# Kernel tuning notes

Hardware: AMD Instinct MI355X
Metric: run time of the kernel (lower is better)

Reference implementation:

```python
import jax, jax.numpy as jnp
import numpy as np

H, W = 224, 224
NF, IN_NF, NL = 32, 100, 4


def conv2d(x, w):
    # 3x3 same-padding conv, NCHW / OIHW
    return jax.lax.conv_general_dilated(x, w, (1, 1), [(1, 1), (1, 1)],
                                        dimension_numbers=('NCHW', 'OIHW', 'NCHW'))


def prelu(x, a):
    return jnp.where(x >= 0, x, a[None, :, None, None] * x)


def bilinear_warp(x, flow):
    # backward warp: sample x at (grid + flow), border clamping
    B, C, Hh, Ww = x.shape
    yy, xx = jnp.meshgrid(jnp.arange(Hh, dtype=x.dtype), jnp.arange(Ww, dtype=x.dtype), indexing='ij')
    px = xx[None] + flow[:, 0]  # [B,H,W]
    py = yy[None] + flow[:, 1]
    x0 = jnp.floor(px); y0 = jnp.floor(py)
    wx = (px - x0)[:, None]; wy = (py - y0)[:, None]  # [B,1,H,W]
    cx = lambda v: jnp.clip(v, 0, Ww - 1).astype(jnp.int32)
    cy = lambda v: jnp.clip(v, 0, Hh - 1).astype(jnp.int32)
    x0i, x1i = cx(x0), cx(x0 + 1)
    y0i, y1i = cy(y0), cy(y0 + 1)
    gather = jax.vmap(lambda img, yi, xi: img[:, yi, xi])  # per-batch fancy gather -> [C,H,W]
    I00 = gather(x, y0i, x0i); I01 = gather(x, y0i, x1i)
    I10 = gather(x, y1i, x0i); I11 = gather(x, y1i, x1i)
    return I00 * (1 - wx) * (1 - wy) + I01 * wx * (1 - wy) + I10 * (1 - wx) * wy + I11 * wx * wy


def glblock_forward(feat_0, feat_1, feat_dense, flow, space_mask,
                    w_head, a_head, w_blocks, a_blocks, w_last, b_last, w_mask, b_mask):
    f0w = bilinear_warp(feat_0, flow[:, :2])
    f1w = bilinear_warp(feat_1, flow[:, 2:4])
    x = jnp.concatenate([f0w, f1w, feat_dense, flow], axis=1)  # [1, in_nf, H, W]
    mask_up = jnp.repeat(jnp.repeat(space_mask, 2, axis=2), 2, axis=3)
    # head: conv3x3 (no bias) + PReLU, then spatial masking
    x = prelu(conv2d(x, w_head), a_head) * space_mask
    outs = [x]
    for i in range(w_blocks.shape[0]):
        x = prelu(conv2d(x, w_blocks[i]) * space_mask, a_blocks[i])
        outs.append(x)
    feats = jnp.concatenate(outs, axis=1)  # [1, in_nf*(NL+1), H, W]
    x = jnp.einsum('oi,bihw->bohw', w_last, feats) + b_last[None, :, None, None]  # 1x1 conv
    smn = conv2d(x[:, 4:], w_mask) + b_mask[None, :, None, None]  # [1,2,H,W]
    B, C, Hh, Ww = x.shape
    xu = jax.image.resize(x, (B, C, 2 * Hh, 2 * Ww), 'linear')
    smnu = jax.image.resize(smn, (B, 2, 2 * Hh, 2 * Ww), 'linear')
    flow_out = xu[:, :4]
    feat_t = xu[:, 4:]
    # eval-mode hard routing mask (training uses gumbel-softmax)
    mask_next = (smnu[:, :1] > smnu[:, 1:]).astype(x.dtype) * mask_up
    return flow_out, feat_t, mask_next


def setup_inputs() -> dict:
    key = jax.random.key(0)
    ks = jax.random.split(key, 12)
    r = lambda i, shape, s=1.0: jax.random.normal(ks[i], shape, jnp.float32) * s
    return {
        'feat_0': r(0, (1, NF, H, W)),
        'feat_1': r(1, (1, NF, H, W)),
        'feat_dense': r(2, (1, NF, H, W)),
        'flow': r(3, (1, 4, H, W)),
        'space_mask': jax.random.uniform(ks[4], (1, 1, H, W), jnp.float32),
        'w_head': r(5, (IN_NF, IN_NF, 3, 3), 0.02),
        'a_head': jnp.full((IN_NF,), 0.25, jnp.float32),
        'w_blocks': r(6, (NL, IN_NF, IN_NF, 3, 3), 0.02),
        'a_blocks': jnp.full((NL, IN_NF), 0.25, jnp.float32),
        'w_last': r(7, (4 + NF, IN_NF * (NL + 1)), 0.02),
        'b_last': r(8, (4 + NF,), 0.02),
        'w_mask': r(9, (2, NF, 3, 3), 0.02),
        'b_mask': r(10, (2,), 0.02),
    }


def reference(feat_0, feat_1, feat_dense, flow, space_mask,
              w_head, a_head, w_blocks, a_blocks, w_last, b_last, w_mask, b_mask):
    return glblock_forward(feat_0, feat_1, feat_dense, flow, space_mask,
                           w_head, a_head, w_blocks, a_blocks, w_last, b_last, w_mask, b_mask)
```

## Files before the change

### kernel.cpp

```cpp
#include <hip/hip_runtime.h>
#include <hip/hip_bf16.h>

#define HWs 50176
#define WID 224
#define OHW 200704

typedef __attribute__((ext_vector_type(8))) short s16x8;
typedef __attribute__((ext_vector_type(4))) float f32x4;

static __device__ __forceinline__ unsigned short f2bf(float x) {
  unsigned u = __float_as_uint(x);
  unsigned r = (u + 0x7fffu + ((u >> 16) & 1u)) >> 16;
  return (unsigned short)r;
}
static __device__ __forceinline__ float bf2f(unsigned short b) {
  return __uint_as_float(((unsigned)b) << 16);
}

__global__ void k_wt(const float* __restrict__ w_head, const float* __restrict__ w_blk,
                     unsigned short* __restrict__ bw) {
  int gid = blockIdx.x * 256 + threadIdx.x;
  int frag = gid >> 7, rr = gid & 127;
  int spl = rr >> 6, lane = rr & 63;
  int l = frag / 288, q = frag - l * 288;
  int t = q / 32, q2 = q - t * 32;
  int ck = q2 >> 3, nt = q2 & 7;
  int oc = nt * 16 + (lane & 15);
  int kg = lane >> 4;
  const float* src = (l == 0) ? w_head : (w_blk + (size_t)(l - 1) * 90000);
  s16x8 outv;
  #pragma unroll
  for (int e = 0; e < 8; ++e) {
    int ic = ck * 32 + kg * 8 + e;
    float w = (oc < 100 && ic < 100) ? src[oc * 900 + ic * 9 + t] : 0.f;
    unsigned short h = f2bf(w);
    unsigned short lo = f2bf(w - bf2f(h));
    outv[e] = (short)(spl ? lo : h);
  }
  ((s16x8*)bw)[gid] = outv;
}

__global__ void k_wlT(const float* __restrict__ wlast, float* __restrict__ wlT) {
  int i = blockIdx.x * 256 + threadIdx.x;
  if (i < 18000) {
    int il = i / 36, o = i - il * 36;
    wlT[i] = wlast[o * 500 + il];
  }
}

__global__ void k_binit(const float* __restrict__ blast, float* __restrict__ xlast) {
  int p = blockIdx.x * 256 + threadIdx.x;
  xlast[(size_t)blockIdx.y * HWs + p] = blast[blockIdx.y];
}

__global__ void k_warp(const float* __restrict__ f0, const float* __restrict__ f1,
                       const float* __restrict__ fd, const float* __restrict__ fl,
                       float* __restrict__ xin) {
  int p = blockIdx.x * 256 + threadIdx.x;
  int yq = blockIdx.y;
  int y = p / WID, x = p - y * WID;
  float fx0 = fl[p];
  float fy0 = fl[HWs + p];
  float fx1 = fl[2 * HWs + p];
  float fy1 = fl[3 * HWs + p];

  #pragma unroll
  for (int img = 0; img < 2; ++img) {
    const float* src = img ? f1 : f0;
    float fx = img ? fx1 : fx0;
    float fy = img ? fy1 : fy0;
    float px = (float)x + fx, py = (float)y + fy;
    float x0f = floorf(px), y0f = floorf(py);
    float wx = px - x0f, wy = py - y0f;
    int x0 = (int)fminf(fmaxf(x0f,       0.f), 223.f);
    int x1 = (int)fminf(fmaxf(x0f + 1.f, 0.f), 223.f);
    int y0 = (int)fminf(fmaxf(y0f,       0.f), 223.f);
    int y1 = (int)fminf(fmaxf(y0f + 1.f, 0.f), 223.f);
    float w00 = (1.f - wx) * (1.f - wy), w01 = wx * (1.f - wy);
    float w10 = (1.f - wx) * wy,         w11 = wx * wy;
    int i00 = y0 * WID + x0, i01 = y0 * WID + x1;
    int i10 = y1 * WID + x0, i11 = y1 * WID + x1;
    float* dst = xin + img * 32 * HWs;
    for (int c = yq * 8; c < yq * 8 + 8; ++c) {
      const float* pl = src + c * HWs;
      dst[c * HWs + p] = w00 * pl[i00] + w01 * pl[i01]
                       + w10 * pl[i10] + w11 * pl[i11];
    }
  }
  for (int c = yq * 8; c < yq * 8 + 8; ++c)
    xin[(64 + c) * HWs + p] = fd[c * HWs + p];
  if (yq == 0) {
    xin[96 * HWs + p] = fx0; xin[97 * HWs + p] = fy0;
    xin[98 * HWs + p] = fx1; xin[99 * HWs + p] = fy1;
  }
}

__global__ __launch_bounds__(256) void k_conv(
    const float* __restrict__ in, const unsigned short* __restrict__ bw,
    const float* __restrict__ avec, const float* __restrict__ mask,
    float* __restrict__ out) {
  __shared__ __align__(16) unsigned char sh[2][6 * 34 * 160];
  const int tid = threadIdx.x;
  const int lane = tid & 63;
  const int wv = tid >> 6;
  const int wr = wv >> 1, wz = wv & 1;
  const int c0 = blockIdx.x * 32;
  const int r0 = blockIdx.y * 4;
  const int li = lane & 15, kg = lane >> 4;

  f32x4 acc[4][4];
  #pragma unroll
  for (int a = 0; a < 4; ++a)
    #pragma unroll
    for (int b = 0; b < 4; ++b) acc[a][b] = (f32x4){0.f, 0.f, 0.f, 0.f};

  const s16x8* bp = (const s16x8*)bw;
  s16x8 bcur[4][2], bnxt[4][2];
  #pragma unroll
  for (int nt = 0; nt < 4; ++nt)
    #pragma unroll
    for (int sp = 0; sp < 2; ++sp)
      bnxt[nt][sp] = bp[(((wz * 4 + nt) * 2 + sp) << 6) + lane];

  auto STAGE = [&](int ck, unsigned char* dst) {
    for (int j = tid; j < 816; j += 256) {
      int kgs = j & 3;
      int rc = j >> 2;
      int pr = rc / 34, pc = rc - pr * 34;
      int gy = r0 - 1 + pr, gx = c0 - 1 + pc;
      int gb = ck * 32 + kgs * 8;
      bool inb = ((unsigned)gy < 224u) && ((unsigned)gx < 224u);
      const float* src = in + (size_t)gb * HWs + gy * WID + gx;
      s16x8 hv, lv;
      #pragma unroll
      for (int e = 0; e < 8; ++e) {
        float v = 0.f;
        if (inb && (gb + e) < 100) v = src[(size_t)e * HWs];
        unsigned short h = f2bf(v);
        unsigned short l2 = f2bf(v - bf2f(h));
        hv[e] = (short)h; lv[e] = (short)l2;
      }
      int base = rc * 160, sw = (rc & 7) << 4;
      *(s16x8*)(dst + base + ((kgs * 16) ^ sw)) = hv;
      *(s16x8*)(dst + base + ((64 + kgs * 16) ^ sw)) = lv;
    }
  };

  STAGE(0, sh[0]);
  __syncthreads();

  for (int ck = 0; ck < 4; ++ck) {
    unsigned char* cur = sh[ck & 1];
    if (ck < 3) STAGE(ck + 1, sh[(ck + 1) & 1]);

    #pragma unroll
    for (int t = 0; t < 9; ++t) {
      #pragma unroll
      for (int nt = 0; nt < 4; ++nt) {
        bcur[nt][0] = bnxt[nt][0];
        bcur[nt][1] = bnxt[nt][1];
      }
      if (t < 8 || ck < 3) {
        int nf = (t < 8) ? (t + 1) * 32 + ck * 8 : (ck + 1) * 8;
        #pragma unroll
        for (int nt = 0; nt < 4; ++nt)
          #pragma unroll
          for (int sp = 0; sp < 2; ++sp)
            bnxt[nt][sp] = bp[(((nf + wz * 4 + nt) * 2 + sp) << 6) + lane];
      }
      const int dy = t / 3 - 1, dx = t - (t / 3) * 3 - 1;
      #pragma unroll
      for (int ms = 0; ms < 4; ++ms) {
        int pr = wr * 2 + (ms >> 1) + 1 + dy;
        int pc = (ms & 1) * 16 + li + 1 + dx;
        int rc = pr * 34 + pc;
        int base = rc * 160, sw = (rc & 7) << 4;
        s16x8 ah = *(const s16x8*)(cur + base + ((kg * 16) ^ sw));
        s16x8 al = *(const s16x8*)(cur + base + ((64 + kg * 16) ^ sw));
        #pragma unroll
        for (int nt = 0; nt < 4; ++nt) {
          acc[ms][nt] = __builtin_amdgcn_mfma_f32_16x16x32_bf16(ah, bcur[nt][0], acc[ms][nt], 0, 0, 0);
          acc[ms][nt] = __builtin_amdgcn_mfma_f32_16x16x32_bf16(al, bcur[nt][0], acc[ms][nt], 0, 0, 0);
          acc[ms][nt] = __builtin_amdgcn_mfma_f32_16x16x32_bf16(ah, bcur[nt][1], acc[ms][nt], 0, 0, 0);
        }
      }
    }
    __syncthreads();
  }

  float4 mv[4];
  #pragma unroll
  for (int ms = 0; ms < 4; ++ms) {
    int row = r0 + wr * 2 + (ms >> 1);
    int colb = c0 + (ms & 1) * 16 + kg * 4;
    mv[ms] = *(const float4*)&mask[row * WID + colb];
  }
  #pragma unroll
  for (int nt = 0; nt < 4; ++nt) {
    int oc = wz * 64 + nt * 16 + li;
    if (oc < 100) {
      float a = avec[oc];
      #pragma unroll
      for (int ms = 0; ms < 4; ++ms) {
        int row = r0 + wr * 2 + (ms >> 1);
        int colb = c0 + (ms & 1) * 16 + kg * 4;
        f32x4 zv = acc[ms][nt];
        float4 o;
        o.x = (zv.x >= 0.f ? zv.x : a * zv.x) * mv[ms].x;
        o.y = (zv.y >= 0.f ? zv.y : a * zv.y) * mv[ms].y;
        o.z = (zv.z >= 0.f ? zv.z : a * zv.z) * mv[ms].z;
        o.w = (zv.w >= 0.f ? zv.w : a * zv.w) * mv[ms].w;
        *(float4*)&out[(size_t)oc * HWs + row * WID + colb] = o;
      }
    }
  }
}

__global__ __launch_bounds__(64) void k_esum(
    const float* __restrict__ A0, const float* __restrict__ A1,
    const float* __restrict__ A2, const float* __restrict__ A3,
    const float* __restrict__ A4, const float* __restrict__ wlT,
    float* __restrict__ xlast) {
  int p = blockIdx.x * 64 + threadIdx.x;
  int l = blockIdx.y;
  const float* a = (l == 0) ? A0 : (l == 1) ? A1 : (l == 2) ? A2 : (l == 3) ? A3 : A4;
  const float* w = wlT + l * 3600;
  float acc[36];
  #pragma unroll
  for (int o = 0; o < 36; ++o) acc[o] = 0.f;
  for (int c0 = 0; c0 < 100; c0 += 10) {
    float v[10];
    #pragma unroll
    for (int q = 0; q < 10; ++q)
      v[q] = a[(size_t)(c0 + q) * HWs + p];
    #pragma unroll
    for (int q = 0; q < 10; ++q) {
      const float4* wp = (const float4*)(w + (c0 + q) * 36);
      #pragma unroll
      for (int j = 0; j < 9; ++j) {
        float4 t = wp[j];
        acc[4*j]   = fmaf(t.x, v[q], acc[4*j]);
        acc[4*j+1] = fmaf(t.y, v[q], acc[4*j+1]);
        acc[4*j+2] = fmaf(t.z, v[q], acc[4*j+2]);
        acc[4*j+3] = fmaf(t.w, v[q], acc[4*j+3]);
      }
    }
  }
  #pragma unroll
  for (int o = 0; o < 36; ++o)
    atomicAdd(&xlast[(size_t)o * HWs + p], acc[o]);
}

__global__ void k_smn(const float* __restrict__ xlast, const float* __restrict__ wmask,
                      const float* __restrict__ bmask, float* __restrict__ smnh) {
  __shared__ float wm[288];
  int tid = threadIdx.x;
  int h = blockIdx.y;
  for (int j = tid; j < 288; j += 64) {
    int o = j / 144, r = j - o * 144;
    wm[j] = wmask[o * 288 + h * 144 + r];
  }
  __syncthreads();
  int p = blockIdx.x * 64 + tid;
  int y = p / WID, x = p - y * WID;
  double a0 = 0.0, a1 = 0.0;
  for (int icl = 0; icl < 16; ++icl) {
    const float* pl = xlast + (size_t)(4 + h * 16 + icl) * HWs;
    #pragma unroll
    for (int dy = -1; dy <= 1; ++dy) {
      int gy = y + dy;
      if ((unsigned)gy < 224u) {
        #pragma unroll
        for (int dx = -1; dx <= 1; ++dx) {
          int gx = x + dx;
          if ((unsigned)gx < 224u) {
            double v = (double)pl[gy * WID + gx];
            int t = (dy + 1) * 3 + (dx + 1);
            a0 += (double)wm[icl * 9 + t] * v;
            a1 += (double)wm[144 + icl * 9 + t] * v;
          }
        }
      }
    }
  }
  if (h == 0) { a0 += (double)bmask[0]; a1 += (double)bmask[1]; }
  smnh[(size_t)(h * 2 + 0) * HWs + p] = (float)a0;
  smnh[(size_t)(h * 2 + 1) * HWs + p] = (float)a1;
}

__global__ void k_upsample(const float* __restrict__ xlast, const float* __restrict__ smnh,
                           const float* __restrict__ smask, float* __restrict__ out) {
  int q = blockIdx.x * 256 + threadIdx.x;
  int oy = q / 448, ox = q - oy * 448;
  int ky = oy >> 1, kx = ox >> 1;
  int r0, r1, c0, c1; float wy0, wy1, wx0, wx1;
  if (oy & 1) { r0 = ky; r1 = (ky < 223) ? ky + 1 : 223; wy0 = 0.75f; wy1 = 0.25f; }
  else        { r0 = (ky > 0) ? ky - 1 : 0; r1 = ky;     wy0 = 0.25f; wy1 = 0.75f; }
  if (ox & 1) { c0 = kx; c1 = (kx < 223) ? kx + 1 : 223; wx0 = 0.75f; wx1 = 0.25f; }
  else        { c0 = (kx > 0) ? kx - 1 : 0; c1 = kx;     wx0 = 0.25f; wx1 = 0.75f; }
  float w00 = wy0 * wx0, w01 = wy0 * wx1, w10 = wy1 * wx0, w11 = wy1 * wx1;
  int i00 = r0 * WID + c0, i01 = r0 * WID + c1, i10 = r1 * WID + c0, i11 = r1 * WID + c1;
  for (int ch = 0; ch < 36; ++ch) {
    const float* pl = xlast + (size_t)ch * HWs;
    out[(size_t)ch * OHW + q] = w00 * pl[i00] + w01 * pl[i01]
                              + w10 * pl[i10] + w11 * pl[i11];
  }
  const float* sa0 = smnh;
  const float* sa1 = smnh + HWs;
  const float* sb0 = smnh + 2 * HWs;
  const float* sb1 = smnh + 3 * HWs;
  double s0 = (double)w00 * ((double)sa0[i00] + (double)sb0[i00])
            + (double)w01 * ((double)sa0[i01] + (double)sb0[i01])
            + (double)w10 * ((double)sa0[i10] + (double)sb0[i10])
            + (double)w11 * ((double)sa0[i11] + (double)sb0[i11]);
  double s1 = (double)w00 * ((double)sa1[i00] + (double)sb1[i00])
            + (double)w01 * ((double)sa1[i01] + (double)sb1[i01])
            + (double)w10 * ((double)sa1[i10] + (double)sb1[i10])
            + (double)w11 * ((double)sa1[i11] + (double)sb1[i11]);
  float mu = smask[ky * WID + kx];
  out[36 * OHW + q] = (s0 > s1) ? mu : 0.f;
}

extern "C" void kernel_launch(void* const* d_in, const int* in_sizes, int n_in,
                              void* d_out, int out_size, void* d_ws, size_t ws_size,
                              hipStream_t stream) {
  const float* feat0   = (const float*)d_in[0];
  const float* feat1   = (const float*)d_in[1];
  const float* featd   = (const float*)d_in[2];
  const float* flow    = (const float*)d_in[3];
  const float* smask   = (const float*)d_in[4];
  const float* w_head  = (const float*)d_in[5];
  const float* a_head  = (const float*)d_in[6];
  const float* w_blk   = (const float*)d_in[7];
  const float* a_blk   = (const float*)d_in[8];
  const float* w_last  = (const float*)d_in[9];
  const float* b_last  = (const float*)d_in[10];
  const float* w_mask  = (const float*)d_in[11];
  const float* b_mask  = (const float*)d_in[12];

  float* B0 = (float*)d_ws;
  float* B1 = B0 + (size_t)100 * HWs;
  float* B2 = B1 + (size_t)100 * HWs;
  float* B3 = B2 + (size_t)100 * HWs;
  float* B4 = B3 + (size_t)100 * HWs;
  float* smnh = B4 + (size_t)100 * HWs;
  float* wlT  = smnh + (size_t)4 * HWs;
  float* xlast = wlT + 18000;
  unsigned short* bw = (unsigned short*)xlast;

  k_wt<<<dim3(720), 256, 0, stream>>>(w_head, w_blk, bw);
  k_wlT<<<dim3(71), 256, 0, stream>>>(w_last, wlT);
  k_warp<<<dim3(196, 4), 256, 0, stream>>>(feat0, feat1, featd, flow, B0);

  dim3 cgrid(7, 56);
  k_conv<<<cgrid, 256, 0, stream>>>(B0, bw,               a_head,      smask, B1);
  k_conv<<<cgrid, 256, 0, stream>>>(B1, bw + 1 * 294912,  a_blk,       smask, B0);
  k_conv<<<cgrid, 256, 0, stream>>>(B0, bw + 2 * 294912,  a_blk + 100, smask, B2);
  k_conv<<<cgrid, 256, 0, stream>>>(B2, bw + 3 * 294912,  a_blk + 200, smask, B3);
  k_conv<<<cgrid, 256, 0, stream>>>(B3, bw + 4 * 294912,  a_blk + 300, smask, B4);

  k_binit<<<dim3(196, 36), 256, 0, stream>>>(b_last, xlast);
  k_esum<<<dim3(784, 5), 64, 0, stream>>>(B1, B0, B2, B3, B4, wlT, xlast);

  k_smn<<<dim3(784, 2), 64, 0, stream>>>(xlast, w_mask, b_mask, smnh);
  k_upsample<<<784, 256, 0, stream>>>(xlast, smnh, smask, (float*)d_out);
}
```

Before: 462.7 us.

## Fuse 1x1 last-conv accumulation into each 3x3 conv epilogue

Each conv layer now stages its activated output tile in shared memory and immediately multiplies it by that layer's slice of the 1x1 last-conv weights, atomically accumulating into xlast. This removes the separate k_esum pass that re-read all five 100-channel activation buffers from global memory, and lets the workspace ping-pong between two buffers. In exchange the conv epilogue does extra FMA work, per-thread global weight loads and 36 atomics per pixel per layer, and uses a larger shared-memory footprint.

```diff
diff --git a/kernel.cpp b/kernel.cpp
--- a/kernel.cpp
+++ b/kernel.cpp
@@ -42,9 +42,10 @@
 
 __global__ void k_wlT(const float* __restrict__ wlast, float* __restrict__ wlT) {
   int i = blockIdx.x * 256 + threadIdx.x;
-  if (i < 18000) {
-    int il = i / 36, o = i - il * 36;
-    wlT[i] = wlast[o * 500 + il];
+  if (i < 18720) {
+    int l = i / 3744, rem = i - l * 3744;
+    int c = rem / 36, o = rem - c * 36;
+    wlT[i] = (c < 100) ? wlast[o * 500 + l * 100 + c] : 0.f;
   }
 }
 
@@ -98,8 +99,9 @@
 __global__ __launch_bounds__(256) void k_conv(
     const float* __restrict__ in, const unsigned short* __restrict__ bw,
     const float* __restrict__ avec, const float* __restrict__ mask,
-    float* __restrict__ out) {
-  __shared__ __align__(16) unsigned char sh[2][6 * 34 * 160];
+    const float* __restrict__ wl, float* __restrict__ out,
+    float* __restrict__ xlast) {
+  __shared__ __align__(16) unsigned char sh[65280];
   const int tid = threadIdx.x;
   const int lane = tid & 63;
   const int wv = tid >> 6;
@@ -146,12 +148,12 @@
     }
   };
 
-  STAGE(0, sh[0]);
+  STAGE(0, sh);
   __syncthreads();
 
   for (int ck = 0; ck < 4; ++ck) {
-    unsigned char* cur = sh[ck & 1];
-    if (ck < 3) STAGE(ck + 1, sh[(ck + 1) & 1]);
+    unsigned char* cur = sh + (ck & 1) * 32640;
+    if (ck < 3) STAGE(ck + 1, sh + ((ck + 1) & 1) * 32640);
 
     #pragma unroll
     for (int t = 0; t < 9; ++t) {
@@ -188,6 +190,7 @@
     __syncthreads();
   }
 
+  float* act = (float*)sh;
   float4 mv[4];
   #pragma unroll
   for (int ms = 0; ms < 4; ++ms) {
@@ -204,6 +207,7 @@
       for (int ms = 0; ms < 4; ++ms) {
         int row = r0 + wr * 2 + (ms >> 1);
         int colb = c0 + (ms & 1) * 16 + kg * 4;
+        int pxb = (wr * 2 + (ms >> 1)) * 32 + (ms & 1) * 16 + kg * 4;
         f32x4 zv = acc[ms][nt];
         float4 o;
         o.x = (zv.x >= 0.f ? zv.x : a * zv.x) * mv[ms].x;
@@ -211,44 +215,51 @@
         o.z = (zv.z >= 0.f ? zv.z : a * zv.z) * mv[ms].z;
         o.w = (zv.w >= 0.f ? zv.w : a * zv.w) * mv[ms].w;
         *(float4*)&out[(size_t)oc * HWs + row * WID + colb] = o;
-      }
-    }
-  }
-}
-
-__global__ __launch_bounds__(64) void k_esum(
-    const float* __restrict__ A0, const float* __restrict__ A1,
-    const float* __restrict__ A2, const float* __restrict__ A3,
-    const float* __restrict__ A4, const float* __restrict__ wlT,
-    float* __restrict__ xlast) {
-  int p = blockIdx.x * 64 + threadIdx.x;
-  int l = blockIdx.y;
-  const float* a = (l == 0) ? A0 : (l == 1) ? A1 : (l == 2) ? A2 : (l == 3) ? A3 : A4;
-  const float* w = wlT + l * 3600;
-  float acc[36];
-  #pragma unroll
-  for (int o = 0; o < 36; ++o) acc[o] = 0.f;
-  for (int c0 = 0; c0 < 100; c0 += 10) {
-    float v[10];
-    #pragma unroll
-    for (int q = 0; q < 10; ++q)
-      v[q] = a[(size_t)(c0 + q) * HWs + p];
-    #pragma unroll
-    for (int q = 0; q < 10; ++q) {
-      const float4* wp = (const float4*)(w + (c0 + q) * 36);
-      #pragma unroll
-      for (int j = 0; j < 9; ++j) {
-        float4 t = wp[j];
-        acc[4*j]   = fmaf(t.x, v[q], acc[4*j]);
-        acc[4*j+1] = fmaf(t.y, v[q], acc[4*j+1]);
-        acc[4*j+2] = fmaf(t.z, v[q], acc[4*j+2]);
-        acc[4*j+3] = fmaf(t.w, v[q], acc[4*j+3]);
-      }
-    }
-  }
+        act[(pxb + 0) * 108 + oc] = o.x;
+        act[(pxb + 1) * 108 + oc] = o.y;
+        act[(pxb + 2) * 108 + oc] = o.z;
+        act[(pxb + 3) * 108 + oc] = o.w;
+      }
+    } else if (oc < 104) {
+      #pragma unroll
+      for (int ms = 0; ms < 4; ++ms) {
+        int pxb = (wr * 2 + (ms >> 1)) * 32 + (ms & 1) * 16 + kg * 4;
+        act[(pxb + 0) * 108 + oc] = 0.f;
+        act[(pxb + 1) * 108 + oc] = 0.f;
+        act[(pxb + 2) * 108 + oc] = 0.f;
+        act[(pxb + 3) * 108 + oc] = 0.f;
+      }
+    }
+  }
+  __syncthreads();
+
+  int px = tid >> 1, h = tid & 1;
+  float ac[36];
+  #pragma unroll
+  for (int o = 0; o < 36; ++o) ac[o] = 0.f;
+  #pragma unroll
+  for (int j = 0; j < 13; ++j) {
+    int c = h * 52 + 4 * j;
+    float4 v4 = *(const float4*)&act[px * 108 + c];
+    float ve[4] = {v4.x, v4.y, v4.z, v4.w};
+    #pragma unroll
+    for (int e = 0; e < 4; ++e) {
+      float v = ve[e];
+      const float4* wp = (const float4*)(wl + (c + e) * 36);
+      #pragma unroll
+      for (int q = 0; q < 9; ++q) {
+        float4 t = wp[q];
+        ac[4*q]   = fmaf(t.x, v, ac[4*q]);
+        ac[4*q+1] = fmaf(t.y, v, ac[4*q+1]);
+        ac[4*q+2] = fmaf(t.z, v, ac[4*q+2]);
+        ac[4*q+3] = fmaf(t.w, v, ac[4*q+3]);
+      }
+    }
+  }
+  int gp = (r0 + (px >> 5)) * WID + c0 + (px & 31);
   #pragma unroll
   for (int o = 0; o < 36; ++o)
-    atomicAdd(&xlast[(size_t)o * HWs + p], acc[o]);
+    atomicAdd(&xlast[(size_t)o * HWs + gp], ac[o]);
 }
 
 __global__ void k_smn(const float* __restrict__ xlast, const float* __restrict__ wmask,
@@ -338,29 +349,24 @@
   const float* w_mask  = (const float*)d_in[11];
   const float* b_mask  = (const float*)d_in[12];
 
-  float* B0 = (float*)d_ws;
-  float* B1 = B0 + (size_t)100 * HWs;
-  float* B2 = B1 + (size_t)100 * HWs;
-  float* B3 = B2 + (size_t)100 * HWs;
-  float* B4 = B3 + (size_t)100 * HWs;
-  float* smnh = B4 + (size_t)100 * HWs;
-  float* wlT  = smnh + (size_t)4 * HWs;
-  float* xlast = wlT + 18000;
-  unsigned short* bw = (unsigned short*)xlast;
+  float* B0    = (float*)d_ws;
+  float* B1    = B0 + (size_t)100 * HWs;
+  float* xlast = B1 + (size_t)100 * HWs;
+  float* smnh  = xlast + (size_t)36 * HWs;
+  float* wlT   = smnh + (size_t)4 * HWs;
+  unsigned short* bw = (unsigned short*)(wlT + 18720);
 
   k_wt<<<dim3(720), 256, 0, stream>>>(w_head, w_blk, bw);
-  k_wlT<<<dim3(71), 256, 0, stream>>>(w_last, wlT);
+  k_wlT<<<dim3(74), 256, 0, stream>>>(w_last, wlT);
+  k_binit<<<dim3(196, 36), 256, 0, stream>>>(b_last, xlast);
   k_warp<<<dim3(196, 4), 256, 0, stream>>>(feat0, feat1, featd, flow, B0);
 
   dim3 cgrid(7, 56);
-  k_conv<<<cgrid, 256, 0, stream>>>(B0, bw,               a_head,      smask, B1);
-  k_conv<<<cgrid, 256, 0, stream>>>(B1, bw + 1 * 294912,  a_blk,       smask, B0);
-  k_conv<<<cgrid, 256, 0, stream>>>(B0, bw + 2 * 294912,  a_blk + 100, smask, B2);
-  k_conv<<<cgrid, 256, 0, stream>>>(B2, bw + 3 * 294912,  a_blk + 200, smask, B3);
-  k_conv<<<cgrid, 256, 0, stream>>>(B3, bw + 4 * 294912,  a_blk + 300, smask, B4);
-
-  k_binit<<<dim3(196, 36), 256, 0, stream>>>(b_last, xlast);
-  k_esum<<<dim3(784, 5), 64, 0, stream>>>(B1, B0, B2, B3, B4, wlT, xlast);
+  k_conv<<<cgrid, 256, 0, stream>>>(B0, bw,              a_head,      smask, wlT,            B1, xlast);
+  k_conv<<<cgrid, 256, 0, stream>>>(B1, bw + 1 * 294912, a_blk,       smask, wlT + 1 * 3744, B0, xlast);
+  k_conv<<<cgrid, 256, 0, stream>>>(B0, bw + 2 * 294912, a_blk + 100, smask, wlT + 2 * 3744, B1, xlast);
+  k_conv<<<cgrid, 256, 0, stream>>>(B1, bw + 3 * 294912, a_blk + 200, smask, wlT + 3 * 3744, B0, xlast);
+  k_conv<<<cgrid, 256, 0, stream>>>(B0, bw + 4 * 294912, a_blk + 300, smask, wlT + 4 * 3744, B1, xlast);
 
   k_smn<<<dim3(784, 2), 64, 0, stream>>>(xlast, w_mask, b_mask, smnh);
   k_upsample<<<784, 256, 0, stream>>>(xlast, smnh, smask, (float*)d_out);
```

New measurement: 892.5 us. 1.93x slower.
